# Performance work log

Measured on AMD Instinct MI355X. Metric: run time of the kernel, lower is better.

Reference implementation:

```python
import math
import jax, jax.numpy as jnp
import numpy as np

NUM_EXPERTS = 8
CAPACITY_FACTOR = 1.5

def setup_inputs() -> dict:
    key = jax.random.key(0)
    ks = jax.random.split(key, 4)
    B, T, D, F, E = 4, 2048, 1024, 4096, NUM_EXPERTS
    scale = 0.02
    return {
        "x": jax.random.normal(ks[0], (B, T, D), dtype=jnp.float32),
        "router_w": jax.random.normal(ks[1], (E, D), dtype=jnp.float32) * scale,  # nn.Linear(D,E,bias=False).weight
        "w1": jax.random.normal(ks[2], (E, D, F), dtype=jnp.float32) * scale,
        "b1": jnp.zeros((E, F), dtype=jnp.float32),
        "w2": jax.random.normal(ks[3], (E, F, D), dtype=jnp.float32) * scale,
        "b2": jnp.zeros((E, D), dtype=jnp.float32),
    }

def reference(x, router_w, w1, b1, w2, b2):
    B, T, D = x.shape
    E = router_w.shape[0]
    N = B * T
    C = max(math.ceil(CAPACITY_FACTOR * N / E), 1)  # static per-expert capacity

    x_flat = x.reshape(N, D)
    logits = x_flat @ router_w.T                      # [N, E]
    probs = jax.nn.softmax(logits, axis=-1)
    chosen_e = jnp.argmax(probs, axis=-1)             # [N] int
    chosen_p = jnp.max(probs, axis=-1)                # [N]

    # First-come-first-served capacity: position of each token within its expert's queue
    onehot = jax.nn.one_hot(chosen_e, E, dtype=jnp.float32)          # [N, E]
    pos = jnp.take_along_axis(jnp.cumsum(onehot, axis=0), chosen_e[:, None], axis=1)[:, 0] - 1.0
    pos = pos.astype(jnp.int32)                                       # [N]
    kept = (pos < C)                                                  # [N] bool
    pos_c = jnp.clip(pos, 0, C - 1)

    # Scatter tokens into per-expert capacity buffers [E, C, D]; dropped tokens contribute 0
    buf = jnp.zeros((E, C, D), dtype=x.dtype).at[chosen_e, pos_c].add(
        x_flat * kept[:, None].astype(x.dtype))

    # Expert FFN: Linear -> exact GELU -> Linear (torch nn.GELU default = erf)
    h = jax.nn.gelu(jnp.einsum('ecd,edf->ecf', buf, w1) + b1[:, None, :], approximate=False)
    eo = jnp.einsum('ecf,efd->ecd', h, w2) + b2[:, None, :]           # [E, C, D]

    # Gather back and scale by router prob; dropped tokens get zeros
    y = eo[chosen_e, pos_c] * (chosen_p * kept.astype(x.dtype))[:, None]
    return y.reshape(B, T, D)
```

## Files before the change

kernel.cpp:

```cpp
#include <hip/hip_runtime.h>
#include <hip/hip_bf16.h>
#include <math.h>

typedef unsigned short u16;
typedef __attribute__((ext_vector_type(8))) short short8;
typedef __attribute__((ext_vector_type(4))) float f32x4;

#define NTOK 8192
#define DMODEL 1024
#define FDIM 4096
#define NEXP 8
#define CAP 1536

__device__ __forceinline__ u16 f2bf(float f) {
  __hip_bfloat16 b = __float2bfloat16(f);
  u16 u;
  __builtin_memcpy(&u, &b, 2);
  return u;
}

__device__ __forceinline__ float gelu_exact(float v) {
  float x = v * 0.70710678118654752f;
  float ax = fabsf(x);
  float t = __builtin_amdgcn_rcpf(1.0f + 0.3275911f * ax);
  float p =
      t * (0.254829592f +
           t * (-0.284496736f +
                t * (1.421413741f + t * (-1.453152027f + t * 1.061405429f))));
  float er = 1.0f - p * __expf(-ax * ax);
  er = copysignf(er, x);
  return 0.5f * v * (1.0f + er);
}

__device__ __forceinline__ void gload_lds16(const u16* g, u16* l) {
  __builtin_amdgcn_global_load_lds(
      (const __attribute__((address_space(1))) void*)g,
      (__attribute__((address_space(3))) void*)l, 16, 0, 0);
}

__global__ __launch_bounds__(256) void router_cast_kernel(
    const float* __restrict__ x, const float* __restrict__ rw,
    u16* __restrict__ xbf, int* __restrict__ chosen_e,
    float* __restrict__ chosen_p) {
  int b = blockIdx.x, tid = threadIdx.x;
  if (b < 4096) {
    size_t base = (size_t)b * 2048 + tid * 8;
    float4 v0 = *(const float4*)(x + base);
    float4 v1 = *(const float4*)(x + base + 4);
    short8 sv;
    sv[0] = (short)f2bf(v0.x); sv[1] = (short)f2bf(v0.y);
    sv[2] = (short)f2bf(v0.z); sv[3] = (short)f2bf(v0.w);
    sv[4] = (short)f2bf(v1.x); sv[5] = (short)f2bf(v1.y);
    sv[6] = (short)f2bf(v1.z); sv[7] = (short)f2bf(v1.w);
    *(short8*)(xbf + base) = sv;
  } else {
    int tok = ((b - 4096) * 256 + tid) >> 6;
    int lane = tid & 63;
    const float4* xp = (const float4*)(x + (size_t)tok * DMODEL) + lane * 4;
    float4 x0 = xp[0], x1 = xp[1], x2 = xp[2], x3 = xp[3];
    float l[8];
#pragma unroll
    for (int e = 0; e < 8; e++) {
      const float4* wp = (const float4*)(rw + (size_t)e * DMODEL) + lane * 4;
      float4 w0 = wp[0], w1v = wp[1], w2v = wp[2], w3 = wp[3];
      float s = x0.x * w0.x + x0.y * w0.y + x0.z * w0.z + x0.w * w0.w;
      s += x1.x * w1v.x + x1.y * w1v.y + x1.z * w1v.z + x1.w * w1v.w;
      s += x2.x * w2v.x + x2.y * w2v.y + x2.z * w2v.z + x2.w * w2v.w;
      s += x3.x * w3.x + x3.y * w3.y + x3.z * w3.z + x3.w * w3.w;
      l[e] = s;
    }
#pragma unroll
    for (int off = 32; off > 0; off >>= 1) {
#pragma unroll
      for (int e = 0; e < 8; e++) l[e] += __shfl_xor(l[e], off, 64);
    }
    if (lane == 0) {
      float best = l[0];
      int am = 0;
#pragma unroll
      for (int e = 1; e < 8; e++)
        if (l[e] > best) { best = l[e]; am = e; }
      float denom = 0.f;
#pragma unroll
      for (int e = 0; e < 8; e++) denom += expf(l[e] - best);
      chosen_e[tok] = am;
      chosen_p[tok] = 1.0f / denom;
    }
  }
}

__device__ __forceinline__ void trans256(const float* __restrict__ ip,
                                         u16* __restrict__ op, int Rin,
                                         int Cin, int r0, int c0, char* lds,
                                         int tid) {
  int w = tid >> 6, l = tid & 63;
#pragma unroll
  for (int i = 0; i < 16; i++) {
    int row = w * 16 + i;
    float4 v = *(const float4*)(ip + (size_t)(r0 + row) * Cin + c0 + l * 4);
    uint2 d;
    d.x = (unsigned)f2bf(v.x) | ((unsigned)f2bf(v.y) << 16);
    d.y = (unsigned)f2bf(v.z) | ((unsigned)f2bf(v.w) << 16);
    int ch = (l >> 1) ^ ((row >> 3) & 7);
    *(uint2*)(lds + row * 512 + ch * 16 + (l & 1) * 8) = d;
  }
  __syncthreads();
#pragma unroll
  for (int p = 0; p < 2; p++) {
    int c = ((tid >> 5) + p * 32) * 4;
    int rb = (tid & 31) * 8;
    short8 s0, s1, s2, s3;
#pragma unroll
    for (int j = 0; j < 8; j++) {
      int r = rb + j;
      int ch = (c >> 3) ^ ((r >> 3) & 7);
      uint2 d = *(const uint2*)(lds + r * 512 + ch * 16 + (c & 7) * 2);
      s0[j] = (short)(d.x & 0xffff);
      s1[j] = (short)(d.x >> 16);
      s2[j] = (short)(d.y & 0xffff);
      s3[j] = (short)(d.y >> 16);
    }
    u16* ob = op + (size_t)(c0 + c) * Rin + r0 + rb;
    *(short8*)(ob) = s0;
    *(short8*)(ob + (size_t)Rin) = s1;
    *(short8*)(ob + 2 * (size_t)Rin) = s2;
    *(short8*)(ob + 3 * (size_t)Rin) = s3;
  }
}

__global__ __launch_bounds__(1024, 1) void wtrans_kernel(
    const float* __restrict__ w1, const float* __restrict__ w2,
    u16* __restrict__ w1t, u16* __restrict__ w2t,
    const int* __restrict__ chosen_e, int* __restrict__ tok_of_slot,
    int* __restrict__ counts, float* __restrict__ out) {
  extern __shared__ char lds[];
  int b = blockIdx.x, tid = threadIdx.x;
  if (b == 0) {
    if (tid < 512) {
      int w = tid >> 6, lane = tid & 63;
      unsigned long long ltmask =
          (lane == 63) ? ~0ull >> 1 : (1ull << lane) - 1ull;
      int cnt = 0;
      for (int c = 0; c < NTOK / 64; c++) {
        int i = c * 64 + lane;
        int e = chosen_e[i];
        unsigned long long bal = __ballot(e == w);
        if (e == w) {
          int p = cnt + __popcll(bal & ltmask);
          if (p < CAP) {
            tok_of_slot[w * CAP + p] = i;
          } else {
            float4 z = make_float4(0.f, 0.f, 0.f, 0.f);
            float* orow = out + (size_t)i * DMODEL;
            for (int d = 0; d < DMODEL; d += 4) *(float4*)(orow + d) = z;
          }
        }
        cnt += __popcll(bal);
      }
      for (int p = cnt + lane; p < CAP; p += 64) tok_of_slot[w * CAP + p] = -1;
      if (lane == 0) counts[w] = cnt < CAP ? cnt : CAP;
    }
  } else if (b < 513) {
    int idx = b - 1;
    int e = idx >> 6, rem = idx & 63;
    int r0 = (rem >> 4) * 256, c0 = (rem & 15) * 256;
    trans256(w1 + (size_t)e * DMODEL * FDIM, w1t + (size_t)e * DMODEL * FDIM,
             DMODEL, FDIM, r0, c0, lds, tid);
  } else {
    int idx = b - 513;
    int e = idx >> 6, rem = idx & 63;
    int r0 = (rem >> 2) * 256, c0 = (rem & 3) * 256;
    trans256(w2 + (size_t)e * DMODEL * FDIM, w2t + (size_t)e * DMODEL * FDIM,
             FDIM, DMODEL, r0, c0, lds, tid);
  }
}

template <int NX, int NY>
__device__ __forceinline__ void tile_coords(int& bx, int& by, int& bz) {
  int flat = blockIdx.x + NX * (blockIdx.y + NY * blockIdx.z);
  int nwg = NX * NY * (int)gridDim.z;
  int swz = (flat & 7) * (nwg >> 3) + (flat >> 3);
  bx = swz % NX;
  int rem = swz / NX;
  by = rem % NY;
  bz = rem / NY;
}

template <int KD>
__device__ __forceinline__ void mainloop_db(const u16* pa0, const u16* pa1,
                                            const u16* pb0, const u16* pb1,
                                            u16* smem, f32x4 (&acc)[4][4],
                                            int tid) {
  int wid = tid >> 6, lane = tid & 63;
  int wm = (wid >> 1) * 64, wn = (wid & 1) * 64;
  int fr = lane & 15, fk = (lane >> 4) * 8;
  int aro = (wm + fr) * 32 + fk;
  int bro = 4096 + (wn + fr) * 32 + fk;
  gload_lds16(pa0, smem + tid * 8);
  gload_lds16(pa1, smem + 2048 + tid * 8);
  gload_lds16(pb0, smem + 4096 + tid * 8);
  gload_lds16(pb1, smem + 6144 + tid * 8);
  __syncthreads();
  int cur = 0;
#pragma unroll 1
  for (int t = 0; t < KD / 32; ++t) {
    const u16* cb = smem + cur * 8192;
    u16* nb = smem + (cur ^ 1) * 8192;
    if (t + 1 < KD / 32) {
      int k = (t + 1) * 32;
      gload_lds16(pa0 + k, nb + tid * 8);
      gload_lds16(pa1 + k, nb + 2048 + tid * 8);
      gload_lds16(pb0 + k, nb + 4096 + tid * 8);
      gload_lds16(pb1 + k, nb + 6144 + tid * 8);
    }
    short8 av[4], bv[4];
#pragma unroll
    for (int m = 0; m < 4; m++) av[m] = *(const short8*)(cb + aro + m * 512);
#pragma unroll
    for (int n = 0; n < 4; n++) bv[n] = *(const short8*)(cb + bro + n * 512);
#pragma unroll
    for (int m = 0; m < 4; m++)
#pragma unroll
      for (int n = 0; n < 4; n++)
        acc[m][n] = __builtin_amdgcn_mfma_f32_16x16x32_bf16(av[m], bv[n],
                                                            acc[m][n], 0, 0, 0);
    __syncthreads();
    cur ^= 1;
  }
}

template <int NX, int NY>
__global__ __launch_bounds__(256) void gemm1_kernel(
    const u16* __restrict__ xbf, const u16* __restrict__ w1tB,
    const int* __restrict__ tok_of_slot, const int* __restrict__ counts,
    u16* __restrict__ hB, const float* __restrict__ b1, int e0,
    long long hStrideE) {
  __shared__ __align__(16) u16 smem[16384];
  int bx, by, bz;
  tile_coords<NX, NY>(bx, by, bz);
  int e = e0 + bz;
  int m0 = by * 128, n0 = bx * 128;
  if (m0 >= counts[e]) return;
  const u16* Bg = w1tB + (size_t)e * FDIM * DMODEL;
  u16* H = hB + (size_t)bz * hStrideE;
  const float* b1g = b1 + (size_t)e * FDIM;
  int tid = threadIdx.x;
  int r2 = tid >> 2, c8 = (tid & 3) * 8;
  int t0 = tok_of_slot[e * CAP + m0 + r2];
  t0 &= ~(t0 >> 31);
  int t1 = tok_of_slot[e * CAP + m0 + 64 + r2];
  t1 &= ~(t1 >> 31);
  const u16* pa0 = xbf + (size_t)t0 * DMODEL + c8;
  const u16* pa1 = xbf + (size_t)t1 * DMODEL + c8;
  const u16* pb0 = Bg + (size_t)(n0 + r2) * DMODEL + c8;
  const u16* pb1 = pb0 + (size_t)64 * DMODEL;
  f32x4 acc[4][4] = {};
  mainloop_db<DMODEL>(pa0, pa1, pb0, pb1, smem, acc, tid);

  int wid = tid >> 6, lane = tid & 63;
  int wm = (wid >> 1) * 64, wn = (wid & 1) * 64;
  int fr = lane & 15, fq = lane >> 4;
  float bias[4];
#pragma unroll
  for (int n = 0; n < 4; n++) bias[n] = b1g[n0 + wn + n * 16 + fr];
#pragma unroll
  for (int m = 0; m < 4; m++) {
#pragma unroll
    for (int n = 0; n < 4; n++) {
      int colL = wn + n * 16 + fr;
#pragma unroll
      for (int j = 0; j < 4; j++) {
        int rL = wm + m * 16 + fq * 4 + j;
        float v = gelu_exact(acc[m][n][j] + bias[n]);
        int ch = (colL >> 3) ^ ((rL >> 2) & 7);
        smem[rL * 128 + ch * 8 + (colL & 7)] = f2bf(v);
      }
    }
  }
  __syncthreads();
#pragma unroll
  for (int p = 0; p < 8; p++) {
    int idx = p * 256 + tid;
    int rr = idx >> 4, cch = idx & 15;
    int ch = cch ^ ((rr >> 2) & 7);
    short8 v = *(const short8*)(smem + rr * 128 + ch * 8);
    *(short8*)(H + (size_t)(m0 + rr) * FDIM + n0 + cch * 8) = v;
  }
}

template <int NX, int NY>
__global__ __launch_bounds__(256) void gemm2_kernel(
    const u16* __restrict__ hB, const u16* __restrict__ w2tB,
    float* __restrict__ out, const float* __restrict__ b2,
    const int* __restrict__ tok_of_slot, const int* __restrict__ counts,
    const float* __restrict__ chosen_p, int e0, long long hStrideE) {
  __shared__ __align__(16) u16 smem[16384];
  int bx, by, bz;
  tile_coords<NX, NY>(bx, by, bz);
  int e = e0 + bz;
  int m0 = by * 128, n0 = bx * 128;
  if (m0 >= counts[e]) return;
  const u16* Ag = hB + (size_t)bz * hStrideE;
  const u16* Bg = w2tB + (size_t)e * DMODEL * FDIM;
  const float* b2g = b2 + (size_t)e * DMODEL;
  int tid = threadIdx.x;
  int r2 = tid >> 2, c8 = (tid & 3) * 8;
  const u16* pa0 = Ag + (size_t)(m0 + r2) * FDIM + c8;
  const u16* pa1 = pa0 + (size_t)64 * FDIM;
  const u16* pb0 = Bg + (size_t)(n0 + r2) * FDIM + c8;
  const u16* pb1 = pb0 + (size_t)64 * FDIM;
  f32x4 acc[4][4] = {};
  mainloop_db<FDIM>(pa0, pa1, pb0, pb1, smem, acc, tid);

  int wid = tid >> 6, lane = tid & 63;
  int wm = (wid >> 1) * 64, wn = (wid & 1) * 64;
  int fr = lane & 15, fq = lane >> 4;
  float bias[4];
#pragma unroll
  for (int n = 0; n < 4; n++) bias[n] = b2g[n0 + wn + n * 16 + fr];
#pragma unroll
  for (int m = 0; m < 4; m++) {
#pragma unroll
    for (int j = 0; j < 4; j++) {
      int rL = wm + m * 16 + fq * 4 + j;
      int tk = tok_of_slot[e * CAP + m0 + rL];
      if (tk >= 0) {
        float sc = chosen_p[tk];
#pragma unroll
        for (int n = 0; n < 4; n++) {
          int colL = wn + n * 16 + fr;
          out[(size_t)tk * DMODEL + n0 + colL] = (acc[m][n][j] + bias[n]) * sc;
        }
      }
    }
  }
}

extern "C" void kernel_launch(void* const* d_in, const int* in_sizes, int n_in,
                              void* d_out, int out_size, void* d_ws,
                              size_t ws_size, hipStream_t stream) {
  const float* x = (const float*)d_in[0];
  const float* rw = (const float*)d_in[1];
  const float* w1 = (const float*)d_in[2];
  const float* b1 = (const float*)d_in[3];
  const float* w2 = (const float*)d_in[4];
  const float* b2 = (const float*)d_in[5];
  float* out = (float*)d_out;

  char* ws = (char*)d_ws;
  size_t off = 0;
  auto alloc = [&](size_t bytes) -> void* {
    void* p = ws + off;
    off = (off + bytes + 255) & ~(size_t)255;
    return p;
  };
  int* chosen_e = (int*)alloc((size_t)NTOK * 4);
  float* chosen_p = (float*)alloc((size_t)NTOK * 4);
  int* tok_of_slot = (int*)alloc((size_t)NEXP * CAP * 4);
  int* counts = (int*)alloc(NEXP * 4);
  u16* xbf = (u16*)alloc((size_t)NTOK * DMODEL * 2);
  u16* w1t = (u16*)alloc((size_t)NEXP * DMODEL * FDIM * 2);
  u16* w2t = (u16*)alloc((size_t)NEXP * DMODEL * FDIM * 2);
  size_t hFull = (size_t)NEXP * CAP * FDIM * 2;
  size_t hLoop = (size_t)CAP * FDIM * 2;
  bool full = (off + hFull) <= ws_size;
  u16* h = (u16*)alloc(full ? hFull : hLoop);

  static_assert(CAP % 128 == 0 && FDIM % 128 == 0 && DMODEL % 128 == 0, "");
  const int TLDS = 131072;
  hipFuncSetAttribute((const void*)wtrans_kernel,
                      hipFuncAttributeMaxDynamicSharedMemorySize, TLDS);

  router_cast_kernel<<<4096 + NTOK / 4, 256, 0, stream>>>(x, rw, xbf, chosen_e,
                                                          chosen_p);
  wtrans_kernel<<<1025, 1024, TLDS, stream>>>(w1, w2, w1t, w2t, chosen_e,
                                              tok_of_slot, counts, out);

  if (full) {
    gemm1_kernel<FDIM / 128, CAP / 128>
        <<<dim3(FDIM / 128, CAP / 128, NEXP), 256, 0, stream>>>(
            xbf, w1t, tok_of_slot, counts, h, b1, 0, (long long)CAP * FDIM);
    gemm2_kernel<DMODEL / 128, CAP / 128>
        <<<dim3(DMODEL / 128, CAP / 128, NEXP), 256, 0, stream>>>(
            h, w2t, out, b2, tok_of_slot, counts, chosen_p, 0,
            (long long)CAP * FDIM);
  } else {
    for (int e = 0; e < NEXP; e++) {
      gemm1_kernel<FDIM / 128, CAP / 128>
          <<<dim3(FDIM / 128, CAP / 128, 1), 256, 0, stream>>>(
              xbf, w1t, tok_of_slot, counts, h, b1, e, 0);
      gemm2_kernel<DMODEL / 128, CAP / 128>
          <<<dim3(DMODEL / 128, CAP / 128, 1), 256, 0, stream>>>(
              h, w2t, out, b2, tok_of_slot, counts, chosen_p, e, 0);
    }
  }
  (void)in_sizes;
  (void)n_in;
  (void)ws_size;
}
```

Measured before the change: 321.5 us.

## Switch expert GEMMs to 32x32x16 MFMA and widen gemm1 tile to 128x256

```diff
diff --git a/kernel.cpp b/kernel.cpp
--- a/kernel.cpp
+++ b/kernel.cpp
@@ -4,7 +4,7 @@
 
 typedef unsigned short u16;
 typedef __attribute__((ext_vector_type(8))) short short8;
-typedef __attribute__((ext_vector_type(4))) float f32x4;
+typedef __attribute__((ext_vector_type(16))) float f32x16;
 
 #define NTOK 8192
 #define DMODEL 1024
@@ -186,60 +186,19 @@
   bz = rem / NY;
 }
 
-template <int KD>
-__device__ __forceinline__ void mainloop_db(const u16* pa0, const u16* pa1,
-                                            const u16* pb0, const u16* pb1,
-                                            u16* smem, f32x4 (&acc)[4][4],
-                                            int tid) {
-  int wid = tid >> 6, lane = tid & 63;
-  int wm = (wid >> 1) * 64, wn = (wid & 1) * 64;
-  int fr = lane & 15, fk = (lane >> 4) * 8;
-  int aro = (wm + fr) * 32 + fk;
-  int bro = 4096 + (wn + fr) * 32 + fk;
-  gload_lds16(pa0, smem + tid * 8);
-  gload_lds16(pa1, smem + 2048 + tid * 8);
-  gload_lds16(pb0, smem + 4096 + tid * 8);
-  gload_lds16(pb1, smem + 6144 + tid * 8);
-  __syncthreads();
-  int cur = 0;
-#pragma unroll 1
-  for (int t = 0; t < KD / 32; ++t) {
-    const u16* cb = smem + cur * 8192;
-    u16* nb = smem + (cur ^ 1) * 8192;
-    if (t + 1 < KD / 32) {
-      int k = (t + 1) * 32;
-      gload_lds16(pa0 + k, nb + tid * 8);
-      gload_lds16(pa1 + k, nb + 2048 + tid * 8);
-      gload_lds16(pb0 + k, nb + 4096 + tid * 8);
-      gload_lds16(pb1 + k, nb + 6144 + tid * 8);
-    }
-    short8 av[4], bv[4];
-#pragma unroll
-    for (int m = 0; m < 4; m++) av[m] = *(const short8*)(cb + aro + m * 512);
-#pragma unroll
-    for (int n = 0; n < 4; n++) bv[n] = *(const short8*)(cb + bro + n * 512);
-#pragma unroll
-    for (int m = 0; m < 4; m++)
-#pragma unroll
-      for (int n = 0; n < 4; n++)
-        acc[m][n] = __builtin_amdgcn_mfma_f32_16x16x32_bf16(av[m], bv[n],
-                                                            acc[m][n], 0, 0, 0);
-    __syncthreads();
-    cur ^= 1;
-  }
-}
+#define ROWMAP(r, kh) (((r)&3) + 8 * ((r) >> 2) + 4 * (kh))
 
 template <int NX, int NY>
-__global__ __launch_bounds__(256) void gemm1_kernel(
+__global__ __launch_bounds__(256, 2) void gemm1_kernel(
     const u16* __restrict__ xbf, const u16* __restrict__ w1tB,
     const int* __restrict__ tok_of_slot, const int* __restrict__ counts,
     u16* __restrict__ hB, const float* __restrict__ b1, int e0,
     long long hStrideE) {
-  __shared__ __align__(16) u16 smem[16384];
+  __shared__ __align__(16) u16 smem[24576];
   int bx, by, bz;
   tile_coords<NX, NY>(bx, by, bz);
   int e = e0 + bz;
-  int m0 = by * 128, n0 = bx * 128;
+  int m0 = by * 128, n0 = bx * 256;
   if (m0 >= counts[e]) return;
   const u16* Bg = w1tB + (size_t)e * FDIM * DMODEL;
   u16* H = hB + (size_t)bz * hStrideE;
@@ -254,42 +213,93 @@
   const u16* pa1 = xbf + (size_t)t1 * DMODEL + c8;
   const u16* pb0 = Bg + (size_t)(n0 + r2) * DMODEL + c8;
   const u16* pb1 = pb0 + (size_t)64 * DMODEL;
-  f32x4 acc[4][4] = {};
-  mainloop_db<DMODEL>(pa0, pa1, pb0, pb1, smem, acc, tid);
+  const u16* pb2 = pb0 + (size_t)128 * DMODEL;
+  const u16* pb3 = pb0 + (size_t)192 * DMODEL;
 
   int wid = tid >> 6, lane = tid & 63;
-  int wm = (wid >> 1) * 64, wn = (wid & 1) * 64;
-  int fr = lane & 15, fq = lane >> 4;
+  int wm = (wid >> 1) * 64, wn = (wid & 1) * 128;
+  int il = lane & 31, kh = lane >> 5;
+  int abase = (wm + il) * 32 + kh * 8;
+  int bbase = 4096 + (wn + il) * 32 + kh * 8;
+  f32x16 acc[2][4] = {};
+
+  gload_lds16(pa0, smem + tid * 8);
+  gload_lds16(pa1, smem + 2048 + tid * 8);
+  gload_lds16(pb0, smem + 4096 + tid * 8);
+  gload_lds16(pb1, smem + 6144 + tid * 8);
+  gload_lds16(pb2, smem + 8192 + tid * 8);
+  gload_lds16(pb3, smem + 10240 + tid * 8);
+  __syncthreads();
+  int cur = 0;
+#pragma unroll 1
+  for (int t = 0; t < DMODEL / 32; ++t) {
+    const u16* cb = smem + cur * 12288;
+    u16* nb = smem + (cur ^ 1) * 12288;
+    if (t + 1 < DMODEL / 32) {
+      int k = (t + 1) * 32;
+      gload_lds16(pa0 + k, nb + tid * 8);
+      gload_lds16(pa1 + k, nb + 2048 + tid * 8);
+      gload_lds16(pb0 + k, nb + 4096 + tid * 8);
+      gload_lds16(pb1 + k, nb + 6144 + tid * 8);
+      gload_lds16(pb2 + k, nb + 8192 + tid * 8);
+      gload_lds16(pb3 + k, nb + 10240 + tid * 8);
+    }
+#pragma unroll
+    for (int kk = 0; kk < 2; kk++) {
+      short8 av[2], bv[4];
+#pragma unroll
+      for (int m = 0; m < 2; m++)
+        av[m] = *(const short8*)(cb + abase + m * 1024 + kk * 16);
+#pragma unroll
+      for (int n = 0; n < 4; n++)
+        bv[n] = *(const short8*)(cb + bbase + n * 1024 + kk * 16);
+#pragma unroll
+      for (int m = 0; m < 2; m++)
+#pragma unroll
+        for (int n = 0; n < 4; n++)
+          acc[m][n] = __builtin_amdgcn_mfma_f32_32x32x16_bf16(
+              av[m], bv[n], acc[m][n], 0, 0, 0);
+    }
+    __syncthreads();
+    cur ^= 1;
+  }
+
   float bias[4];
 #pragma unroll
-  for (int n = 0; n < 4; n++) bias[n] = b1g[n0 + wn + n * 16 + fr];
-#pragma unroll
-  for (int m = 0; m < 4; m++) {
-#pragma unroll
-    for (int n = 0; n < 4; n++) {
-      int colL = wn + n * 16 + fr;
-#pragma unroll
-      for (int j = 0; j < 4; j++) {
-        int rL = wm + m * 16 + fq * 4 + j;
-        float v = gelu_exact(acc[m][n][j] + bias[n]);
-        int ch = (colL >> 3) ^ ((rL >> 2) & 7);
-        smem[rL * 128 + ch * 8 + (colL & 7)] = f2bf(v);
+  for (int n = 0; n < 4; n++) bias[n] = b1g[n0 + wn + n * 32 + il];
+#pragma unroll
+  for (int half = 0; half < 2; half++) {
+    if ((wid >> 1) == half) {
+#pragma unroll
+      for (int m = 0; m < 2; m++) {
+#pragma unroll
+        for (int n = 0; n < 4; n++) {
+          int col = wn + n * 32 + il;
+#pragma unroll
+          for (int r = 0; r < 16; r++) {
+            int rL = m * 32 + ROWMAP(r, kh);
+            float v = gelu_exact(acc[m][n][r] + bias[n]);
+            int ch = (col >> 3) ^ ((rL >> 2) & 7);
+            smem[rL * 256 + ch * 8 + (col & 7)] = f2bf(v);
+          }
+        }
       }
     }
-  }
-  __syncthreads();
-#pragma unroll
-  for (int p = 0; p < 8; p++) {
-    int idx = p * 256 + tid;
-    int rr = idx >> 4, cch = idx & 15;
-    int ch = cch ^ ((rr >> 2) & 7);
-    short8 v = *(const short8*)(smem + rr * 128 + ch * 8);
-    *(short8*)(H + (size_t)(m0 + rr) * FDIM + n0 + cch * 8) = v;
+    __syncthreads();
+#pragma unroll
+    for (int p = 0; p < 8; p++) {
+      int idx = p * 256 + tid;
+      int rr = idx >> 5, cch = idx & 31;
+      int ch = cch ^ ((rr >> 2) & 7);
+      short8 v = *(const short8*)(smem + rr * 256 + ch * 8);
+      *(short8*)(H + (size_t)(m0 + half * 64 + rr) * FDIM + n0 + cch * 8) = v;
+    }
+    __syncthreads();
   }
 }
 
 template <int NX, int NY>
-__global__ __launch_bounds__(256) void gemm2_kernel(
+__global__ __launch_bounds__(256, 2) void gemm2_kernel(
     const u16* __restrict__ hB, const u16* __restrict__ w2tB,
     float* __restrict__ out, const float* __restrict__ b2,
     const int* __restrict__ tok_of_slot, const int* __restrict__ counts,
@@ -309,27 +319,66 @@
   const u16* pa1 = pa0 + (size_t)64 * FDIM;
   const u16* pb0 = Bg + (size_t)(n0 + r2) * FDIM + c8;
   const u16* pb1 = pb0 + (size_t)64 * FDIM;
-  f32x4 acc[4][4] = {};
-  mainloop_db<FDIM>(pa0, pa1, pb0, pb1, smem, acc, tid);
 
   int wid = tid >> 6, lane = tid & 63;
   int wm = (wid >> 1) * 64, wn = (wid & 1) * 64;
-  int fr = lane & 15, fq = lane >> 4;
-  float bias[4];
-#pragma unroll
-  for (int n = 0; n < 4; n++) bias[n] = b2g[n0 + wn + n * 16 + fr];
-#pragma unroll
-  for (int m = 0; m < 4; m++) {
-#pragma unroll
-    for (int j = 0; j < 4; j++) {
-      int rL = wm + m * 16 + fq * 4 + j;
+  int il = lane & 31, kh = lane >> 5;
+  int abase = (wm + il) * 32 + kh * 8;
+  int bbase = 4096 + (wn + il) * 32 + kh * 8;
+  f32x16 acc[2][2] = {};
+
+  gload_lds16(pa0, smem + tid * 8);
+  gload_lds16(pa1, smem + 2048 + tid * 8);
+  gload_lds16(pb0, smem + 4096 + tid * 8);
+  gload_lds16(pb1, smem + 6144 + tid * 8);
+  __syncthreads();
+  int cur = 0;
+#pragma unroll 1
+  for (int t = 0; t < FDIM / 32; ++t) {
+    const u16* cb = smem + cur * 8192;
+    u16* nb = smem + (cur ^ 1) * 8192;
+    if (t + 1 < FDIM / 32) {
+      int k = (t + 1) * 32;
+      gload_lds16(pa0 + k, nb + tid * 8);
+      gload_lds16(pa1 + k, nb + 2048 + tid * 8);
+      gload_lds16(pb0 + k, nb + 4096 + tid * 8);
+      gload_lds16(pb1 + k, nb + 6144 + tid * 8);
+    }
+#pragma unroll
+    for (int kk = 0; kk < 2; kk++) {
+      short8 av[2], bv[2];
+#pragma unroll
+      for (int m = 0; m < 2; m++)
+        av[m] = *(const short8*)(cb + abase + m * 1024 + kk * 16);
+#pragma unroll
+      for (int n = 0; n < 2; n++)
+        bv[n] = *(const short8*)(cb + bbase + n * 1024 + kk * 16);
+#pragma unroll
+      for (int m = 0; m < 2; m++)
+#pragma unroll
+        for (int n = 0; n < 2; n++)
+          acc[m][n] = __builtin_amdgcn_mfma_f32_32x32x16_bf16(
+              av[m], bv[n], acc[m][n], 0, 0, 0);
+    }
+    __syncthreads();
+    cur ^= 1;
+  }
+
+  float bias[2];
+#pragma unroll
+  for (int n = 0; n < 2; n++) bias[n] = b2g[n0 + wn + n * 32 + il];
+#pragma unroll
+  for (int m = 0; m < 2; m++) {
+#pragma unroll
+    for (int r = 0; r < 16; r++) {
+      int rL = wm + m * 32 + ROWMAP(r, kh);
       int tk = tok_of_slot[e * CAP + m0 + rL];
       if (tk >= 0) {
         float sc = chosen_p[tk];
 #pragma unroll
-        for (int n = 0; n < 4; n++) {
-          int colL = wn + n * 16 + fr;
-          out[(size_t)tk * DMODEL + n0 + colL] = (acc[m][n][j] + bias[n]) * sc;
+        for (int n = 0; n < 2; n++) {
+          int col = wn + n * 32 + il;
+          out[(size_t)tk * DMODEL + n0 + col] = (acc[m][n][r] + bias[n]) * sc;
         }
       }
     }
@@ -366,7 +415,7 @@
   bool full = (off + hFull) <= ws_size;
   u16* h = (u16*)alloc(full ? hFull : hLoop);
 
-  static_assert(CAP % 128 == 0 && FDIM % 128 == 0 && DMODEL % 128 == 0, "");
+  static_assert(CAP % 128 == 0 && FDIM % 256 == 0 && DMODEL % 128 == 0, "");
   const int TLDS = 131072;
   hipFuncSetAttribute((const void*)wtrans_kernel,
                       hipFuncAttributeMaxDynamicSharedMemorySize, TLDS);
@@ -377,8 +426,8 @@
                                               tok_of_slot, counts, out);
 
   if (full) {
-    gemm1_kernel<FDIM / 128, CAP / 128>
-        <<<dim3(FDIM / 128, CAP / 128, NEXP), 256, 0, stream>>>(
+    gemm1_kernel<FDIM / 256, CAP / 128>
+        <<<dim3(FDIM / 256, CAP / 128, NEXP), 256, 0, stream>>>(
             xbf, w1t, tok_of_slot, counts, h, b1, 0, (long long)CAP * FDIM);
     gemm2_kernel<DMODEL / 128, CAP / 128>
         <<<dim3(DMODEL / 128, CAP / 128, NEXP), 256, 0, stream>>>(
@@ -386,8 +435,8 @@
             (long long)CAP * FDIM);
   } else {
     for (int e = 0; e < NEXP; e++) {
-      gemm1_kernel<FDIM / 128, CAP / 128>
-          <<<dim3(FDIM / 128, CAP / 128, 1), 256, 0, stream>>>(
+      gemm1_kernel<FDIM / 256, CAP / 128>
+          <<<dim3(FDIM / 256, CAP / 128, 1), 256, 0, stream>>>(
               xbf, w1t, tok_of_slot, counts, h, b1, e, 0);
       gemm2_kernel<DMODEL / 128, CAP / 128>
           <<<dim3(DMODEL / 128, CAP / 128, 1), 256, 0, stream>>>(
```

New measurement: 362.4 us. 12.7% more time.

## Use three-stage LDS ring buffer with partial vmcnt waits in GEMM mainloop

Applied to the files above, without the earlier changes.

```diff
diff --git a/kernel.cpp b/kernel.cpp
--- a/kernel.cpp
+++ b/kernel.cpp
@@ -11,6 +11,9 @@
 #define FDIM 4096
 #define NEXP 8
 #define CAP 1536
+
+#define VMWAIT(N) asm volatile("s_waitcnt vmcnt(" #N ")" ::: "memory")
+#define BAR __builtin_amdgcn_s_barrier()
 
 __device__ __forceinline__ u16 f2bf(float f) {
   __hip_bfloat16 b = __float2bfloat16(f);
@@ -187,32 +190,25 @@
 }
 
 template <int KD>
-__device__ __forceinline__ void mainloop_db(const u16* pa0, const u16* pa1,
-                                            const u16* pb0, const u16* pb1,
-                                            u16* smem, f32x4 (&acc)[4][4],
-                                            int tid) {
+__device__ __forceinline__ void mainloop_ring3(const u16* pa0, const u16* pa1,
+                                               const u16* pb0, const u16* pb1,
+                                               u16* smem, f32x4 (&acc)[4][4],
+                                               int tid) {
   int wid = tid >> 6, lane = tid & 63;
   int wm = (wid >> 1) * 64, wn = (wid & 1) * 64;
   int fr = lane & 15, fk = (lane >> 4) * 8;
   int aro = (wm + fr) * 32 + fk;
   int bro = 4096 + (wn + fr) * 32 + fk;
-  gload_lds16(pa0, smem + tid * 8);
-  gload_lds16(pa1, smem + 2048 + tid * 8);
-  gload_lds16(pb0, smem + 4096 + tid * 8);
-  gload_lds16(pb1, smem + 6144 + tid * 8);
-  __syncthreads();
-  int cur = 0;
-#pragma unroll 1
-  for (int t = 0; t < KD / 32; ++t) {
-    const u16* cb = smem + cur * 8192;
-    u16* nb = smem + (cur ^ 1) * 8192;
-    if (t + 1 < KD / 32) {
-      int k = (t + 1) * 32;
-      gload_lds16(pa0 + k, nb + tid * 8);
-      gload_lds16(pa1 + k, nb + 2048 + tid * 8);
-      gload_lds16(pb0 + k, nb + 4096 + tid * 8);
-      gload_lds16(pb1 + k, nb + 6144 + tid * 8);
-    }
+  auto stage = [&](int t) {
+    u16* d = smem + (t % 3) * 8192 + tid * 8;
+    int k = t * 32;
+    gload_lds16(pa0 + k, d);
+    gload_lds16(pa1 + k, d + 2048);
+    gload_lds16(pb0 + k, d + 4096);
+    gload_lds16(pb1 + k, d + 6144);
+  };
+  auto compute = [&](int t) {
+    const u16* cb = smem + (t % 3) * 8192;
     short8 av[4], bv[4];
 #pragma unroll
     for (int m = 0; m < 4; m++) av[m] = *(const short8*)(cb + aro + m * 512);
@@ -224,9 +220,24 @@
       for (int n = 0; n < 4; n++)
         acc[m][n] = __builtin_amdgcn_mfma_f32_16x16x32_bf16(av[m], bv[n],
                                                             acc[m][n], 0, 0, 0);
-    __syncthreads();
-    cur ^= 1;
-  }
+  };
+  const int KT = KD / 32;
+  stage(0);
+  stage(1);
+  VMWAIT(4);
+  BAR;
+#pragma unroll 1
+  for (int t = 0; t < KT - 2; ++t) {
+    stage(t + 2);
+    compute(t);
+    VMWAIT(4);
+    BAR;
+  }
+  compute(KT - 2);
+  VMWAIT(0);
+  BAR;
+  compute(KT - 1);
+  BAR;
 }
 
 template <int NX, int NY>
@@ -235,7 +246,7 @@
     const int* __restrict__ tok_of_slot, const int* __restrict__ counts,
     u16* __restrict__ hB, const float* __restrict__ b1, int e0,
     long long hStrideE) {
-  __shared__ __align__(16) u16 smem[16384];
+  __shared__ __align__(16) u16 smem[24576];
   int bx, by, bz;
   tile_coords<NX, NY>(bx, by, bz);
   int e = e0 + bz;
@@ -255,7 +266,7 @@
   const u16* pb0 = Bg + (size_t)(n0 + r2) * DMODEL + c8;
   const u16* pb1 = pb0 + (size_t)64 * DMODEL;
   f32x4 acc[4][4] = {};
-  mainloop_db<DMODEL>(pa0, pa1, pb0, pb1, smem, acc, tid);
+  mainloop_ring3<DMODEL>(pa0, pa1, pb0, pb1, smem, acc, tid);
 
   int wid = tid >> 6, lane = tid & 63;
   int wm = (wid >> 1) * 64, wn = (wid & 1) * 64;
@@ -294,7 +305,7 @@
     float* __restrict__ out, const float* __restrict__ b2,
     const int* __restrict__ tok_of_slot, const int* __restrict__ counts,
     const float* __restrict__ chosen_p, int e0, long long hStrideE) {
-  __shared__ __align__(16) u16 smem[16384];
+  __shared__ __align__(16) u16 smem[24576];
   int bx, by, bz;
   tile_coords<NX, NY>(bx, by, bz);
   int e = e0 + bz;
@@ -310,7 +321,7 @@
   const u16* pb0 = Bg + (size_t)(n0 + r2) * FDIM + c8;
   const u16* pb1 = pb0 + (size_t)64 * FDIM;
   f32x4 acc[4][4] = {};
-  mainloop_db<FDIM>(pa0, pa1, pb0, pb1, smem, acc, tid);
+  mainloop_ring3<FDIM>(pa0, pa1, pb0, pb1, smem, acc, tid);
 
   int wid = tid >> 6, lane = tid & 63;
   int wm = (wid >> 1) * 64, wn = (wid & 1) * 64;
```

After: 344.1 us. 1.07x slower.

## Overlap weight transposes with router and GEMM1 by co-scheduling in shared kernels

Applied to the files above, without the earlier changes.

```diff
diff --git a/kernel.cpp b/kernel.cpp
--- a/kernel.cpp
+++ b/kernel.cpp
@@ -38,104 +38,99 @@
       (__attribute__((address_space(3))) void*)l, 16, 0, 0);
 }
 
-__global__ __launch_bounds__(256) void router_cast_kernel(
-    const float* __restrict__ x, const float* __restrict__ rw,
-    u16* __restrict__ xbf, int* __restrict__ chosen_e,
-    float* __restrict__ chosen_p) {
-  int b = blockIdx.x, tid = threadIdx.x;
-  if (b < 4096) {
-    size_t base = (size_t)b * 2048 + tid * 8;
-    float4 v0 = *(const float4*)(x + base);
-    float4 v1 = *(const float4*)(x + base + 4);
-    short8 sv;
-    sv[0] = (short)f2bf(v0.x); sv[1] = (short)f2bf(v0.y);
-    sv[2] = (short)f2bf(v0.z); sv[3] = (short)f2bf(v0.w);
-    sv[4] = (short)f2bf(v1.x); sv[5] = (short)f2bf(v1.y);
-    sv[6] = (short)f2bf(v1.z); sv[7] = (short)f2bf(v1.w);
-    *(short8*)(xbf + base) = sv;
-  } else {
-    int tok = ((b - 4096) * 256 + tid) >> 6;
-    int lane = tid & 63;
-    const float4* xp = (const float4*)(x + (size_t)tok * DMODEL) + lane * 4;
-    float4 x0 = xp[0], x1 = xp[1], x2 = xp[2], x3 = xp[3];
-    float l[8];
-#pragma unroll
-    for (int e = 0; e < 8; e++) {
-      const float4* wp = (const float4*)(rw + (size_t)e * DMODEL) + lane * 4;
-      float4 w0 = wp[0], w1v = wp[1], w2v = wp[2], w3 = wp[3];
-      float s = x0.x * w0.x + x0.y * w0.y + x0.z * w0.z + x0.w * w0.w;
-      s += x1.x * w1v.x + x1.y * w1v.y + x1.z * w1v.z + x1.w * w1v.w;
-      s += x2.x * w2v.x + x2.y * w2v.y + x2.z * w2v.z + x2.w * w2v.w;
-      s += x3.x * w3.x + x3.y * w3.y + x3.z * w3.z + x3.w * w3.w;
-      l[e] = s;
-    }
-#pragma unroll
-    for (int off = 32; off > 0; off >>= 1) {
-#pragma unroll
-      for (int e = 0; e < 8; e++) l[e] += __shfl_xor(l[e], off, 64);
-    }
-    if (lane == 0) {
-      float best = l[0];
-      int am = 0;
-#pragma unroll
-      for (int e = 1; e < 8; e++)
-        if (l[e] > best) { best = l[e]; am = e; }
-      float denom = 0.f;
-#pragma unroll
-      for (int e = 0; e < 8; e++) denom += expf(l[e] - best);
-      chosen_e[tok] = am;
-      chosen_p[tok] = 1.0f / denom;
-    }
-  }
-}
-
-__device__ __forceinline__ void trans256(const float* __restrict__ ip,
-                                         u16* __restrict__ op, int Rin,
-                                         int Cin, int r0, int c0, char* lds,
-                                         int tid) {
-  int w = tid >> 6, l = tid & 63;
+__device__ __forceinline__ void trans128(const float* __restrict__ ip,
+                                         u16* __restrict__ op, int Cin,
+                                         int ostride, int r0, int c0,
+                                         char* lds, int tid) {
+  int w = tid >> 5, l = tid & 31;
 #pragma unroll
   for (int i = 0; i < 16; i++) {
-    int row = w * 16 + i;
+    int row = i * 8 + w;
     float4 v = *(const float4*)(ip + (size_t)(r0 + row) * Cin + c0 + l * 4);
     uint2 d;
     d.x = (unsigned)f2bf(v.x) | ((unsigned)f2bf(v.y) << 16);
     d.y = (unsigned)f2bf(v.z) | ((unsigned)f2bf(v.w) << 16);
     int ch = (l >> 1) ^ ((row >> 3) & 7);
-    *(uint2*)(lds + row * 512 + ch * 16 + (l & 1) * 8) = d;
+    *(uint2*)(lds + row * 256 + ch * 16 + (l & 1) * 8) = d;
   }
   __syncthreads();
 #pragma unroll
   for (int p = 0; p < 2; p++) {
-    int c = ((tid >> 5) + p * 32) * 4;
-    int rb = (tid & 31) * 8;
+    int c = ((tid >> 4) + p * 16) * 4;
+    int rb = (tid & 15) * 8;
     short8 s0, s1, s2, s3;
 #pragma unroll
     for (int j = 0; j < 8; j++) {
       int r = rb + j;
       int ch = (c >> 3) ^ ((r >> 3) & 7);
-      uint2 d = *(const uint2*)(lds + r * 512 + ch * 16 + (c & 7) * 2);
+      uint2 d = *(const uint2*)(lds + r * 256 + ch * 16 + (c & 7) * 2);
       s0[j] = (short)(d.x & 0xffff);
       s1[j] = (short)(d.x >> 16);
       s2[j] = (short)(d.y & 0xffff);
       s3[j] = (short)(d.y >> 16);
     }
-    u16* ob = op + (size_t)(c0 + c) * Rin + r0 + rb;
+    u16* ob = op + (size_t)(c0 + c) * ostride + r0 + rb;
     *(short8*)(ob) = s0;
-    *(short8*)(ob + (size_t)Rin) = s1;
-    *(short8*)(ob + 2 * (size_t)Rin) = s2;
-    *(short8*)(ob + 3 * (size_t)Rin) = s3;
-  }
-}
-
-__global__ __launch_bounds__(1024, 1) void wtrans_kernel(
-    const float* __restrict__ w1, const float* __restrict__ w2,
-    u16* __restrict__ w1t, u16* __restrict__ w2t,
+    *(short8*)(ob + ostride) = s1;
+    *(short8*)(ob + 2 * (size_t)ostride) = s2;
+    *(short8*)(ob + 3 * (size_t)ostride) = s3;
+  }
+}
+
+__global__ __launch_bounds__(256) void router_w1t_kernel(
+    const float* __restrict__ x, const float* __restrict__ rw,
+    const float* __restrict__ w1, int* __restrict__ chosen_e,
+    float* __restrict__ chosen_p, u16* __restrict__ w1t) {
+  __shared__ __align__(16) char lds[32768];
+  int bid = blockIdx.x, tid = threadIdx.x;
+  if (bid & 1) {
+    int idx = bid >> 1;
+    int e = idx >> 8, rem = idx & 255;
+    int r0 = (rem >> 5) * 128, c0 = (rem & 31) * 128;
+    trans128(w1 + (size_t)e * DMODEL * FDIM, w1t + (size_t)e * DMODEL * FDIM,
+             FDIM, DMODEL, r0, c0, lds, tid);
+    return;
+  }
+  int tok = ((bid >> 1) * 256 + tid) >> 6;
+  int lane = tid & 63;
+  const float4* xp = (const float4*)(x + (size_t)tok * DMODEL) + lane * 4;
+  float4 x0 = xp[0], x1 = xp[1], x2 = xp[2], x3 = xp[3];
+  float l[8];
+#pragma unroll
+  for (int e = 0; e < 8; e++) {
+    const float4* wp = (const float4*)(rw + (size_t)e * DMODEL) + lane * 4;
+    float4 w0 = wp[0], w1v = wp[1], w2v = wp[2], w3 = wp[3];
+    float s = x0.x * w0.x + x0.y * w0.y + x0.z * w0.z + x0.w * w0.w;
+    s += x1.x * w1v.x + x1.y * w1v.y + x1.z * w1v.z + x1.w * w1v.w;
+    s += x2.x * w2v.x + x2.y * w2v.y + x2.z * w2v.z + x2.w * w2v.w;
+    s += x3.x * w3.x + x3.y * w3.y + x3.z * w3.z + x3.w * w3.w;
+    l[e] = s;
+  }
+#pragma unroll
+  for (int off = 32; off > 0; off >>= 1) {
+#pragma unroll
+    for (int e = 0; e < 8; e++) l[e] += __shfl_xor(l[e], off, 64);
+  }
+  if (lane == 0) {
+    float best = l[0];
+    int am = 0;
+#pragma unroll
+    for (int e = 1; e < 8; e++)
+      if (l[e] > best) { best = l[e]; am = e; }
+    float denom = 0.f;
+#pragma unroll
+    for (int e = 0; e < 8; e++) denom += expf(l[e] - best);
+    chosen_e[tok] = am;
+    chosen_p[tok] = 1.0f / denom;
+  }
+}
+
+__global__ __launch_bounds__(1024) void cast_scan_kernel(
+    const float* __restrict__ x, u16* __restrict__ xbf,
     const int* __restrict__ chosen_e, int* __restrict__ tok_of_slot,
     int* __restrict__ counts, float* __restrict__ out) {
-  extern __shared__ char lds[];
-  int b = blockIdx.x, tid = threadIdx.x;
-  if (b == 0) {
+  int bid = blockIdx.x, tid = threadIdx.x;
+  if (bid == 0) {
     if (tid < 512) {
       int w = tid >> 6, lane = tid & 63;
       unsigned long long ltmask =
@@ -160,30 +155,17 @@
       for (int p = cnt + lane; p < CAP; p += 64) tok_of_slot[w * CAP + p] = -1;
       if (lane == 0) counts[w] = cnt < CAP ? cnt : CAP;
     }
-  } else if (b < 513) {
-    int idx = b - 1;
-    int e = idx >> 6, rem = idx & 63;
-    int r0 = (rem >> 4) * 256, c0 = (rem & 15) * 256;
-    trans256(w1 + (size_t)e * DMODEL * FDIM, w1t + (size_t)e * DMODEL * FDIM,
-             DMODEL, FDIM, r0, c0, lds, tid);
-  } else {
-    int idx = b - 513;
-    int e = idx >> 6, rem = idx & 63;
-    int r0 = (rem >> 2) * 256, c0 = (rem & 3) * 256;
-    trans256(w2 + (size_t)e * DMODEL * FDIM, w2t + (size_t)e * DMODEL * FDIM,
-             FDIM, DMODEL, r0, c0, lds, tid);
-  }
-}
-
-template <int NX, int NY>
-__device__ __forceinline__ void tile_coords(int& bx, int& by, int& bz) {
-  int flat = blockIdx.x + NX * (blockIdx.y + NY * blockIdx.z);
-  int nwg = NX * NY * (int)gridDim.z;
-  int swz = (flat & 7) * (nwg >> 3) + (flat >> 3);
-  bx = swz % NX;
-  int rem = swz / NX;
-  by = rem % NY;
-  bz = rem / NY;
+    return;
+  }
+  size_t base = (size_t)(bid - 1) * 8192 + tid * 8;
+  float4 v0 = *(const float4*)(x + base);
+  float4 v1 = *(const float4*)(x + base + 4);
+  short8 sv;
+  sv[0] = (short)f2bf(v0.x); sv[1] = (short)f2bf(v0.y);
+  sv[2] = (short)f2bf(v0.z); sv[3] = (short)f2bf(v0.w);
+  sv[4] = (short)f2bf(v1.x); sv[5] = (short)f2bf(v1.y);
+  sv[6] = (short)f2bf(v1.z); sv[7] = (short)f2bf(v1.w);
+  *(short8*)(xbf + base) = sv;
 }
 
 template <int KD>
@@ -233,18 +215,41 @@
 __global__ __launch_bounds__(256) void gemm1_kernel(
     const u16* __restrict__ xbf, const u16* __restrict__ w1tB,
     const int* __restrict__ tok_of_slot, const int* __restrict__ counts,
-    u16* __restrict__ hB, const float* __restrict__ b1, int e0,
+    u16* __restrict__ hB, const float* __restrict__ b1,
+    const float* __restrict__ w2, u16* __restrict__ w2t, int mode, int e0,
     long long hStrideE) {
   __shared__ __align__(16) u16 smem[16384];
-  int bx, by, bz;
-  tile_coords<NX, NY>(bx, by, bz);
+  int tid = threadIdx.x;
+  int gid = 0, tIdx = -1, gridz = 1;
+  if (mode == 0) {
+    int r = blockIdx.x % 5;
+    if (r < 2) tIdx = (blockIdx.x / 5) * 2 + r;
+    else gid = (blockIdx.x / 5) * 3 + (r - 2);
+    gridz = NEXP;
+  } else if (mode == 1) {
+    tIdx = blockIdx.x;
+  } else {
+    gid = blockIdx.x;
+  }
+  if (tIdx >= 0) {
+    int e = tIdx >> 8, rem = tIdx & 255;
+    int r0 = (rem >> 3) * 128, c0 = (rem & 7) * 128;
+    trans128(w2 + (size_t)e * DMODEL * FDIM, w2t + (size_t)e * DMODEL * FDIM,
+             DMODEL, FDIM, r0, c0, (char*)smem, tid);
+    return;
+  }
+  int nwg = NX * NY * gridz;
+  int swz = (gid & 7) * (nwg >> 3) + (gid >> 3);
+  int bx = swz % NX;
+  int rem2 = swz / NX;
+  int by = rem2 % NY;
+  int bz = rem2 / NY;
   int e = e0 + bz;
   int m0 = by * 128, n0 = bx * 128;
   if (m0 >= counts[e]) return;
   const u16* Bg = w1tB + (size_t)e * FDIM * DMODEL;
   u16* H = hB + (size_t)bz * hStrideE;
   const float* b1g = b1 + (size_t)e * FDIM;
-  int tid = threadIdx.x;
   int r2 = tid >> 2, c8 = (tid & 3) * 8;
   int t0 = tok_of_slot[e * CAP + m0 + r2];
   t0 &= ~(t0 >> 31);
@@ -286,6 +291,17 @@
     short8 v = *(const short8*)(smem + rr * 128 + ch * 8);
     *(short8*)(H + (size_t)(m0 + rr) * FDIM + n0 + cch * 8) = v;
   }
+}
+
+template <int NX, int NY>
+__device__ __forceinline__ void tile_coords(int& bx, int& by, int& bz) {
+  int flat = blockIdx.x + NX * (blockIdx.y + NY * blockIdx.z);
+  int nwg = NX * NY * (int)gridDim.z;
+  int swz = (flat & 7) * (nwg >> 3) + (flat >> 3);
+  bx = swz % NX;
+  int rem = swz / NX;
+  by = rem % NY;
+  bz = rem / NY;
 }
 
 template <int NX, int NY>
@@ -367,28 +383,27 @@
   u16* h = (u16*)alloc(full ? hFull : hLoop);
 
   static_assert(CAP % 128 == 0 && FDIM % 128 == 0 && DMODEL % 128 == 0, "");
-  const int TLDS = 131072;
-  hipFuncSetAttribute((const void*)wtrans_kernel,
-                      hipFuncAttributeMaxDynamicSharedMemorySize, TLDS);
-
-  router_cast_kernel<<<4096 + NTOK / 4, 256, 0, stream>>>(x, rw, xbf, chosen_e,
-                                                          chosen_p);
-  wtrans_kernel<<<1025, 1024, TLDS, stream>>>(w1, w2, w1t, w2t, chosen_e,
-                                              tok_of_slot, counts, out);
+
+  router_w1t_kernel<<<4096, 256, 0, stream>>>(x, rw, w1, chosen_e, chosen_p,
+                                              w1t);
+  cast_scan_kernel<<<1025, 1024, 0, stream>>>(x, xbf, chosen_e, tok_of_slot,
+                                              counts, out);
 
   if (full) {
-    gemm1_kernel<FDIM / 128, CAP / 128>
-        <<<dim3(FDIM / 128, CAP / 128, NEXP), 256, 0, stream>>>(
-            xbf, w1t, tok_of_slot, counts, h, b1, 0, (long long)CAP * FDIM);
+    gemm1_kernel<FDIM / 128, CAP / 128><<<5120, 256, 0, stream>>>(
+        xbf, w1t, tok_of_slot, counts, h, b1, w2, w2t, 0, 0,
+        (long long)CAP * FDIM);
     gemm2_kernel<DMODEL / 128, CAP / 128>
         <<<dim3(DMODEL / 128, CAP / 128, NEXP), 256, 0, stream>>>(
             h, w2t, out, b2, tok_of_slot, counts, chosen_p, 0,
             (long long)CAP * FDIM);
   } else {
+    gemm1_kernel<FDIM / 128, CAP / 128><<<2048, 256, 0, stream>>>(
+        xbf, w1t, tok_of_slot, counts, h, b1, w2, w2t, 1, 0, 0);
     for (int e = 0; e < NEXP; e++) {
       gemm1_kernel<FDIM / 128, CAP / 128>
-          <<<dim3(FDIM / 128, CAP / 128, 1), 256, 0, stream>>>(
-              xbf, w1t, tok_of_slot, counts, h, b1, e, 0);
+          <<<(FDIM / 128) * (CAP / 128), 256, 0, stream>>>(
+              xbf, w1t, tok_of_slot, counts, h, b1, w2, w2t, 2, e, 0);
       gemm2_kernel<DMODEL / 128, CAP / 128>
           <<<dim3(DMODEL / 128, CAP / 128, 1), 256, 0, stream>>>(
               h, w2t, out, b2, tok_of_slot, counts, chosen_p, e, 0);
```

After: 344.5 us. 1.07x slower.
